# Performance work log

Measured on AMD Instinct MI355X. Metric: run time of the kernel, lower is better.

The kernel has to match this reference:

```python
import jax, jax.numpy as jnp
import numpy as np

N = 4000      # number_of_sensors
D_IN = 128    # input feature dim
D_OUT = 128   # output feature dim
E_DIM = 16    # node embedding dim
B = 8         # batch size


def setup_inputs() -> dict:
    key = jax.random.key(0)
    k_x, k_e1, k_e2, k_w = jax.random.split(key, 4)
    x = jax.random.normal(k_x, (B, N, D_IN), dtype=jnp.float32)
    E1 = jax.random.normal(k_e1, (N, E_DIM), dtype=jnp.float32)
    E2 = jax.random.normal(k_e2, (N, E_DIM), dtype=jnp.float32)
    W = jax.random.normal(k_w, (D_IN, D_OUT), dtype=jnp.float32) * (1.0 / np.sqrt(D_IN))
    b = jnp.zeros((D_OUT,), dtype=jnp.float32)
    return {"x": x, "E1": E1, "E2": E2, "W": W, "b": b}


def reference(x, E1, E2, W, b):
    # Adaptive adjacency from node embeddings: A = softmax(relu(E1 @ E2^T), axis=-1)
    logits = jax.nn.relu(jnp.einsum('nd,md->nm', E1, E2))  # [N, N]
    adj = jax.nn.softmax(logits, axis=-1)                  # row-normalized adjacency
    # Graph aggregation then feature transform: relu(A @ X @ W + b)
    agg = jnp.einsum('nm,bmf->bnf', adj, x)                # [B, N, D_IN]
    out = jax.nn.relu(jnp.einsum('bnf,fo->bno', agg, W) + b)  # [B, N, D_OUT]
    return out
```

## Files before the change

### kernel.cpp

```cpp
#include <hip/hip_runtime.h>
#include <hip/hip_bf16.h>

#define NSEN 4000
#define NP   4096
#define DIN  128
#define DOUT 128
#define EDIM 16
#define BATCH 8

typedef __attribute__((ext_vector_type(8))) short bf16x8;
typedef __attribute__((ext_vector_type(4))) float f32x4;

__device__ __forceinline__ unsigned short f2bf(float f) {
  unsigned int u = __float_as_uint(f);
  unsigned int r = (u + 0x7FFFu + ((u >> 16) & 1u)) >> 16;
  return (unsigned short)r;
}
__device__ __forceinline__ float bf2f(unsigned short s) {
  unsigned int u = ((unsigned int)s) << 16;
  return __uint_as_float(u);
}

__device__ __forceinline__ void gl_lds16(const void* g, void* l) {
  __builtin_amdgcn_global_load_lds((const __attribute__((address_space(1))) void*)g,
                                   (__attribute__((address_space(3))) void*)l, 16, 0, 0);
}

__global__ __launch_bounds__(512) void k_adj(const float* __restrict__ E1,
                                             const float* __restrict__ E2,
                                             const float* __restrict__ W,
                                             unsigned short* __restrict__ adjp,
                                             float* __restrict__ rinv,
                                             unsigned short* __restrict__ Wt) {
  __shared__ float rsum[8][16];
  if (blockIdx.x == NSEN / 16) {
    for (int i = threadIdx.x; i < DIN * DOUT; i += 512) {
      int o = i >> 7, f = i & 127;
      Wt[i] = f2bf(W[(size_t)f * DOUT + o]);
    }
    return;
  }
  const int tid = threadIdx.x;
  const int lane = tid & 63, wv = tid >> 6;
  const int lr = lane & 15, lq = lane >> 4;
  const int n0 = blockIdx.x * 16;

  float a[8];
  {
    const float* e1p = &E1[(size_t)(n0 + lr) * EDIM + (lq & 1) * 8];
    *(float4*)&a[0] = *(const float4*)e1p;
    *(float4*)&a[4] = *(const float4*)(e1p + 4);
  }
  bf16x8 af1, af2;
#pragma unroll
  for (int j = 0; j < 8; j++) {
    unsigned short hs = f2bf(a[j]);
    af1[j] = (short)hs;
    float lo = a[j] - bf2f(hs);
    af2[j] = (lq < 2) ? (short)f2bf(lo) : (short)0;
  }

  float rs[4] = {0.f, 0.f, 0.f, 0.f};
  for (int t = wv; t < NSEN / 16; t += 8) {
    const int m = t * 16 + lr;
    float bv[8];
    const float* e2p = &E2[(size_t)m * EDIM + (lq & 1) * 8];
    *(float4*)&bv[0] = *(const float4*)e2p;
    *(float4*)&bv[4] = *(const float4*)(e2p + 4);
    bf16x8 bfrag;
#pragma unroll
    for (int j = 0; j < 8; j++) {
      unsigned short hs = f2bf(bv[j]);
      if (lq < 2) bfrag[j] = (short)hs;
      else        bfrag[j] = (short)f2bf(bv[j] - bf2f(hs));
    }
    f32x4 c = (f32x4){0.f, 0.f, 0.f, 0.f};
    c = __builtin_amdgcn_mfma_f32_16x16x32_bf16(af1, bfrag, c, 0, 0, 0);
    c = __builtin_amdgcn_mfma_f32_16x16x32_bf16(af2, bfrag, c, 0, 0, 0);
#pragma unroll
    for (int i = 0; i < 4; i++) {
      float p = __expf(fmaxf(c[i], 0.f));
      rs[i] += p;
      adjp[(size_t)(n0 + lq * 4 + i) * NP + t * 16 + lr] = f2bf(p);
    }
  }
  for (int i = tid; i < 16 * (NP - NSEN); i += 512) {
    int r = i / (NP - NSEN), c = i % (NP - NSEN);
    adjp[(size_t)(n0 + r) * NP + NSEN + c] = 0;
  }
#pragma unroll
  for (int i = 0; i < 4; i++) {
    rs[i] += __shfl_xor(rs[i], 1, 64);
    rs[i] += __shfl_xor(rs[i], 2, 64);
    rs[i] += __shfl_xor(rs[i], 4, 64);
    rs[i] += __shfl_xor(rs[i], 8, 64);
  }
  if (lr == 0) {
#pragma unroll
    for (int i = 0; i < 4; i++) rsum[wv][lq * 4 + i] = rs[i];
  }
  __syncthreads();
  if (tid < 16) {
    float s = 0.f;
#pragma unroll
    for (int w = 0; w < 8; w++) s += rsum[w][tid];
    rinv[n0 + tid] = 1.0f / s;
  }
}

__global__ __launch_bounds__(256) void k_xpt(const float* __restrict__ x,
                                             unsigned short* __restrict__ xpt) {
  __shared__ unsigned short tile[64][72];
  const int t = threadIdx.x;
  const int m0 = blockIdx.x * 64;
  const int f0 = blockIdx.y * 64;
  const int b  = blockIdx.z;
  const int f4 = t & 15, mrow = t >> 4;
#pragma unroll
  for (int rep = 0; rep < 4; rep++) {
    int ml = mrow + rep * 16;
    int m = m0 + ml;
    float4 v = make_float4(0.f, 0.f, 0.f, 0.f);
    if (m < NSEN) v = *(const float4*)&x[((size_t)b * NSEN + m) * DIN + f0 + f4 * 4];
    tile[f4*4+0][ml] = f2bf(v.x);
    tile[f4*4+1][ml] = f2bf(v.y);
    tile[f4*4+2][ml] = f2bf(v.z);
    tile[f4*4+3][ml] = f2bf(v.w);
  }
  __syncthreads();
  const int seg = t & 7, fl0 = t >> 3;
#pragma unroll
  for (int it = 0; it < 2; it++) {
    int fl = fl0 + it * 32;
    int j = b * DIN + f0 + fl;
    uint4 v = *(const uint4*)&tile[fl][seg * 8];
    *(uint4*)&xpt[(size_t)j * NP + m0 + seg * 8] = v;
  }
}

__global__ __launch_bounds__(256, 2) void k_gemm1(const unsigned short* __restrict__ A,
                                                  const unsigned short* __restrict__ Bt,
                                                  const unsigned short* __restrict__ Wt,
                                                  const float* __restrict__ rinv,
                                                  const float* __restrict__ bias,
                                                  float* __restrict__ out) {
  __shared__ __align__(16) unsigned short smem[36864];
  const int tid = threadIdx.x;
  const int lane = tid & 63, wv = tid >> 6;
  const int wr = wv >> 1, wc = wv & 1;
  const int lr = lane & 15, lq = lane >> 4;
  const int m0 = blockIdx.x * 64;
  const int b  = blockIdx.y;
  const int c0 = b * 128;
  unsigned short* tA0 = smem;
  unsigned short* tB0 = smem + 12288;

  f32x4 acc[2][4];
#pragma unroll
  for (int p = 0; p < 2; p++)
#pragma unroll
    for (int q = 0; q < 4; q++) acc[p][q] = (f32x4){0.f, 0.f, 0.f, 0.f};

#define STAGE(bufi, kb)                                                              \
  {                                                                                  \
    _Pragma("unroll")                                                                \
    for (int s = 0; s < 2; s++) {                                                    \
      int idx = s * 256 + tid;                                                       \
      int row = idx >> 3;                                                            \
      int kc = ((idx & 7) ^ (row & 7)) << 3;                                         \
      gl_lds16(&A[(size_t)(m0 + row) * NP + (kb) + kc], &tA0[(bufi)*4096 + idx*8]);  \
    }                                                                                \
    _Pragma("unroll")                                                                \
    for (int s = 0; s < 4; s++) {                                                    \
      int idx = s * 256 + tid;                                                       \
      int row = idx >> 3;                                                            \
      int kc = ((idx & 7) ^ (row & 7)) << 3;                                         \
      gl_lds16(&Bt[(size_t)(c0 + row) * NP + (kb) + kc], &tB0[(bufi)*8192 + idx*8]); \
    }                                                                                \
  }

  STAGE(0, 0);
  STAGE(1, 64);

  int cur = 0;
  for (int it = 0; it < 64; ++it) {
    if (it < 62) {
      int nb = cur + 2; if (nb >= 3) nb -= 3;
      STAGE(nb, (it + 2) * 64);
      asm volatile("s_waitcnt vmcnt(12)" ::: "memory");
    } else if (it == 62) {
      asm volatile("s_waitcnt vmcnt(6)" ::: "memory");
    } else {
      asm volatile("s_waitcnt vmcnt(0)" ::: "memory");
    }
    __builtin_amdgcn_s_barrier();

    bf16x8 af[2][2], bfr[2][4];
#pragma unroll
    for (int sk = 0; sk < 2; sk++) {
      const int koff = (sk * 32 + lq * 8) ^ ((lr & 7) << 3);
#pragma unroll
      for (int p = 0; p < 2; p++)
        af[sk][p] = *(const bf16x8*)&tA0[cur * 4096 + (wr * 32 + p * 16 + lr) * 64 + koff];
#pragma unroll
      for (int q = 0; q < 4; q++)
        bfr[sk][q] = *(const bf16x8*)&tB0[cur * 8192 + (wc * 64 + q * 16 + lr) * 64 + koff];
    }
    asm volatile("s_waitcnt lgkmcnt(0)" ::: "memory");
    __builtin_amdgcn_sched_barrier(0);
    __builtin_amdgcn_s_setprio(1);
#pragma unroll
    for (int sk = 0; sk < 2; sk++)
#pragma unroll
      for (int p = 0; p < 2; p++)
#pragma unroll
        for (int q = 0; q < 4; q++)
          acc[p][q] = __builtin_amdgcn_mfma_f32_16x16x32_bf16(af[sk][p], bfr[sk][q], acc[p][q], 0, 0, 0);
    __builtin_amdgcn_s_setprio(0);
    __builtin_amdgcn_s_barrier();
    cur = cur + 1; if (cur >= 3) cur = 0;
  }
#undef STAGE

  bf16x8 wf[4][4];
#pragma unroll
  for (int q = 0; q < 4; q++)
#pragma unroll
    for (int ks = 0; ks < 4; ks++)
      wf[q][ks] = *(const bf16x8*)&Wt[(size_t)(wc * 64 + q * 16 + lr) * DIN + ks * 32 + lq * 8];

  unsigned short* eps = smem;
#pragma unroll
  for (int p = 0; p < 2; p++) {
    float rv[4];
#pragma unroll
    for (int i = 0; i < 4; i++)
      rv[i] = rinv[m0 + wr * 32 + p * 16 + lq * 4 + i];
#pragma unroll
    for (int q = 0; q < 4; q++)
#pragma unroll
      for (int i = 0; i < 4; i++)
        eps[(wr * 32 + p * 16 + lq * 4 + i) * 136 + wc * 64 + q * 16 + lr] =
            f2bf(acc[p][q][i] * rv[i]);
  }
  __syncthreads();

  f32x4 acc2[2][4];
#pragma unroll
  for (int p = 0; p < 2; p++)
#pragma unroll
    for (int q = 0; q < 4; q++) acc2[p][q] = (f32x4){0.f, 0.f, 0.f, 0.f};

#pragma unroll
  for (int ks = 0; ks < 4; ks++) {
    bf16x8 a2[2];
#pragma unroll
    for (int p = 0; p < 2; p++)
      a2[p] = *(const bf16x8*)&eps[(wr * 32 + p * 16 + lr) * 136 + ks * 32 + lq * 8];
#pragma unroll
    for (int p = 0; p < 2; p++)
#pragma unroll
      for (int q = 0; q < 4; q++)
        acc2[p][q] = __builtin_amdgcn_mfma_f32_16x16x32_bf16(a2[p], wf[q][ks], acc2[p][q], 0, 0, 0);
  }

#pragma unroll
  for (int p = 0; p < 2; p++)
#pragma unroll
    for (int q = 0; q < 4; q++) {
      const int o = wc * 64 + q * 16 + lr;
      const float bb = bias[o];
#pragma unroll
      for (int i = 0; i < 4; i++) {
        const int n = m0 + wr * 32 + p * 16 + lq * 4 + i;
        if (n < NSEN)
          out[((size_t)b * NSEN + n) * DOUT + o] = fmaxf(acc2[p][q][i] + bb, 0.f);
      }
    }
}

extern "C" void kernel_launch(void* const* d_in, const int* in_sizes, int n_in,
                              void* d_out, int out_size, void* d_ws, size_t ws_size,
                              hipStream_t stream) {
  const float* x    = (const float*)d_in[0];
  const float* E1   = (const float*)d_in[1];
  const float* E2   = (const float*)d_in[2];
  const float* W    = (const float*)d_in[3];
  const float* bias = (const float*)d_in[4];
  float* out = (float*)d_out;

  char* ws = (char*)d_ws;
  unsigned short* adjp = (unsigned short*)(ws);
  unsigned short* xpt  = (unsigned short*)(ws + 33554432);
  unsigned short* wt   = (unsigned short*)(ws + 33554432 + 8388608);
  float*          rinv = (float*)(ws + 33554432 + 8388608 + 32768);

  k_adj<<<dim3(NSEN / 16 + 1), dim3(512), 0, stream>>>(E1, E2, W, adjp, rinv, wt);
  k_xpt<<<dim3(NP / 64, DIN / 64, BATCH), dim3(256), 0, stream>>>(x, xpt);
  k_gemm1<<<dim3(NP / 64, BATCH), dim3(256), 0, stream>>>(adjp, xpt, wt, rinv, bias, out);
}
```

Baseline: 81.54 us.

## Split-K the adjacency GEMM into two halves with a separate reduce-and-project kernel

The main GEMM is split along K into two halves via a third grid dimension, so the launch grows from 8x64 to 2x8x63 blocks, improving CU occupancy on a 256-CU device. Each half writes bf16 partial sums to a workspace. A new finishing kernel adds the two partials, applies the row normalisation and runs the W projection, bias and relu. The pipeline drops from triple to double buffering, and LDS fragment loads are split so the first MFMA group can start early, allowing three blocks per CU. This costs an extra launch, partial-sum traffic and bf16 rounding of the partials. The grid now uses 63 row tiles instead of 64, which skips only padded rows beyond 4000.

```diff
diff --git a/kernel.cpp b/kernel.cpp
--- a/kernel.cpp
+++ b/kernel.cpp
@@ -138,22 +138,21 @@
   }
 }
 
-__global__ __launch_bounds__(256, 2) void k_gemm1(const unsigned short* __restrict__ A,
+__global__ __launch_bounds__(256, 3) void k_gemm1(const unsigned short* __restrict__ A,
                                                   const unsigned short* __restrict__ Bt,
-                                                  const unsigned short* __restrict__ Wt,
-                                                  const float* __restrict__ rinv,
-                                                  const float* __restrict__ bias,
-                                                  float* __restrict__ out) {
-  __shared__ __align__(16) unsigned short smem[36864];
+                                                  unsigned short* __restrict__ part) {
+  __shared__ __align__(16) unsigned short smem[24576];
   const int tid = threadIdx.x;
   const int lane = tid & 63, wv = tid >> 6;
   const int wr = wv >> 1, wc = wv & 1;
   const int lr = lane & 15, lq = lane >> 4;
   const int m0 = blockIdx.x * 64;
   const int b  = blockIdx.y;
+  const int kh = blockIdx.z;
   const int c0 = b * 128;
+  const int kb0 = kh * 2048;
   unsigned short* tA0 = smem;
-  unsigned short* tB0 = smem + 12288;
+  unsigned short* tB0 = smem + 8192;
 
   f32x4 acc[2][4];
 #pragma unroll
@@ -179,48 +178,86 @@
     }                                                                                \
   }
 
-  STAGE(0, 0);
-  STAGE(1, 64);
-
-  int cur = 0;
-  for (int it = 0; it < 64; ++it) {
-    if (it < 62) {
-      int nb = cur + 2; if (nb >= 3) nb -= 3;
-      STAGE(nb, (it + 2) * 64);
-      asm volatile("s_waitcnt vmcnt(12)" ::: "memory");
-    } else if (it == 62) {
+  STAGE(0, kb0);
+
+  for (int it = 0; it < 32; ++it) {
+    const int cur = it & 1;
+    if (it < 31) {
+      STAGE(cur ^ 1, kb0 + (it + 1) * 64);
       asm volatile("s_waitcnt vmcnt(6)" ::: "memory");
     } else {
       asm volatile("s_waitcnt vmcnt(0)" ::: "memory");
     }
     __builtin_amdgcn_s_barrier();
 
-    bf16x8 af[2][2], bfr[2][4];
-#pragma unroll
-    for (int sk = 0; sk < 2; sk++) {
-      const int koff = (sk * 32 + lq * 8) ^ ((lr & 7) << 3);
+    bf16x8 af0[2], bf0[4], af1[2], bf1[4];
+    {
+      const int koff0 = (lq * 8) ^ ((lr & 7) << 3);
 #pragma unroll
       for (int p = 0; p < 2; p++)
-        af[sk][p] = *(const bf16x8*)&tA0[cur * 4096 + (wr * 32 + p * 16 + lr) * 64 + koff];
-#pragma unroll
-      for (int q = 0; q < 4; q++)
-        bfr[sk][q] = *(const bf16x8*)&tB0[cur * 8192 + (wc * 64 + q * 16 + lr) * 64 + koff];
-    }
+        af0[p] = *(const bf16x8*)&tA0[cur * 4096 + (wr * 32 + p * 16 + lr) * 64 + koff0];
+#pragma unroll
+      for (int q = 0; q < 4; q++)
+        bf0[q] = *(const bf16x8*)&tB0[cur * 8192 + (wc * 64 + q * 16 + lr) * 64 + koff0];
+    }
+    __builtin_amdgcn_sched_barrier(0);
+    {
+      const int koff1 = (32 + lq * 8) ^ ((lr & 7) << 3);
+#pragma unroll
+      for (int p = 0; p < 2; p++)
+        af1[p] = *(const bf16x8*)&tA0[cur * 4096 + (wr * 32 + p * 16 + lr) * 64 + koff1];
+#pragma unroll
+      for (int q = 0; q < 4; q++)
+        bf1[q] = *(const bf16x8*)&tB0[cur * 8192 + (wc * 64 + q * 16 + lr) * 64 + koff1];
+    }
+    asm volatile("s_waitcnt lgkmcnt(6)" ::: "memory");
+    __builtin_amdgcn_sched_barrier(0);
+    __builtin_amdgcn_s_setprio(1);
+#pragma unroll
+    for (int p = 0; p < 2; p++)
+#pragma unroll
+      for (int q = 0; q < 4; q++)
+        acc[p][q] = __builtin_amdgcn_mfma_f32_16x16x32_bf16(af0[p], bf0[q], acc[p][q], 0, 0, 0);
     asm volatile("s_waitcnt lgkmcnt(0)" ::: "memory");
     __builtin_amdgcn_sched_barrier(0);
-    __builtin_amdgcn_s_setprio(1);
-#pragma unroll
-    for (int sk = 0; sk < 2; sk++)
-#pragma unroll
-      for (int p = 0; p < 2; p++)
-#pragma unroll
-        for (int q = 0; q < 4; q++)
-          acc[p][q] = __builtin_amdgcn_mfma_f32_16x16x32_bf16(af[sk][p], bfr[sk][q], acc[p][q], 0, 0, 0);
+#pragma unroll
+    for (int p = 0; p < 2; p++)
+#pragma unroll
+      for (int q = 0; q < 4; q++)
+        acc[p][q] = __builtin_amdgcn_mfma_f32_16x16x32_bf16(af1[p], bf1[q], acc[p][q], 0, 0, 0);
     __builtin_amdgcn_s_setprio(0);
     __builtin_amdgcn_s_barrier();
-    cur = cur + 1; if (cur >= 3) cur = 0;
   }
 #undef STAGE
+
+  unsigned short* pdst = part + ((size_t)(kh * BATCH + b) * NP + m0) * DIN;
+#pragma unroll
+  for (int p = 0; p < 2; p++)
+#pragma unroll
+    for (int q = 0; q < 4; q++) {
+      const int col = wc * 64 + q * 16 + lr;
+#pragma unroll
+      for (int i = 0; i < 4; i++) {
+        const int row = wr * 32 + p * 16 + lq * 4 + i;
+        pdst[row * DIN + col] = f2bf(acc[p][q][i]);
+      }
+    }
+}
+
+__global__ __launch_bounds__(256, 2) void k_fin(const unsigned short* __restrict__ part,
+                                                const unsigned short* __restrict__ Wt,
+                                                const float* __restrict__ rinv,
+                                                const float* __restrict__ bias,
+                                                float* __restrict__ out) {
+  __shared__ __align__(16) unsigned short eps[64 * 136];
+  const int tid = threadIdx.x;
+  const int lane = tid & 63, wv = tid >> 6;
+  const int wr = wv >> 1, wc = wv & 1;
+  const int lr = lane & 15, lq = lane >> 4;
+  const int m0 = blockIdx.x * 64;
+  const int b = blockIdx.y;
+  const size_t base = ((size_t)b * NP + m0) * DIN;
+  const size_t khoff = (size_t)BATCH * NP * DIN;
 
   bf16x8 wf[4][4];
 #pragma unroll
@@ -229,19 +266,18 @@
     for (int ks = 0; ks < 4; ks++)
       wf[q][ks] = *(const bf16x8*)&Wt[(size_t)(wc * 64 + q * 16 + lr) * DIN + ks * 32 + lq * 8];
 
-  unsigned short* eps = smem;
-#pragma unroll
-  for (int p = 0; p < 2; p++) {
-    float rv[4];
-#pragma unroll
-    for (int i = 0; i < 4; i++)
-      rv[i] = rinv[m0 + wr * 32 + p * 16 + lq * 4 + i];
-#pragma unroll
-    for (int q = 0; q < 4; q++)
-#pragma unroll
-      for (int i = 0; i < 4; i++)
-        eps[(wr * 32 + p * 16 + lq * 4 + i) * 136 + wc * 64 + q * 16 + lr] =
-            f2bf(acc[p][q][i] * rv[i]);
+#pragma unroll
+  for (int s = 0; s < 4; s++) {
+    int c = s * 256 + tid;
+    int row = c >> 4, col = (c & 15) * 8;
+    bf16x8 p0 = *(const bf16x8*)&part[base + row * DIN + col];
+    bf16x8 p1 = *(const bf16x8*)&part[khoff + base + row * DIN + col];
+    float rv = rinv[m0 + row];
+    unsigned short tmp[8];
+#pragma unroll
+    for (int j = 0; j < 8; j++)
+      tmp[j] = f2bf((bf2f((unsigned short)p0[j]) + bf2f((unsigned short)p1[j])) * rv);
+    *(bf16x8*)&eps[row * 136 + col] = *(bf16x8*)tmp;
   }
   __syncthreads();
 
@@ -294,8 +330,10 @@
   unsigned short* xpt  = (unsigned short*)(ws + 33554432);
   unsigned short* wt   = (unsigned short*)(ws + 33554432 + 8388608);
   float*          rinv = (float*)(ws + 33554432 + 8388608 + 32768);
+  unsigned short* part = (unsigned short*)(ws + 33554432 + 8388608 + 32768 + 16384);
 
   k_adj<<<dim3(NSEN / 16 + 1), dim3(512), 0, stream>>>(E1, E2, W, adjp, rinv, wt);
   k_xpt<<<dim3(NP / 64, DIN / 64, BATCH), dim3(256), 0, stream>>>(x, xpt);
-  k_gemm1<<<dim3(NP / 64, BATCH), dim3(256), 0, stream>>>(adjp, xpt, wt, rinv, bias, out);
-}
+  k_gemm1<<<dim3(63, BATCH, 2), dim3(256), 0, stream>>>(adjp, xpt, part);
+  k_fin<<<dim3(63, BATCH), dim3(256), 0, stream>>>(part, wt, rinv, bias, out);
+}
```

New measurement: 95.15 us. 1.17x slower.

## Use 8-wave blocks with double-buffered LDS and split-K MFMA interleave

Applied to the files above, without the earlier changes.

The main GEMM kernel moves from 4 waves to 8 waves per block, so each wave owns a 32x32 output sub-tile. The LDS pipeline drops from triple to double buffering, which shrinks shared memory and allows more resident blocks. LDS fragment loads are split into two k-halves so MFMAs on the first half can start while the second half is still loading. The trade-off is a shallower global prefetch (one stage ahead instead of two) and more barrier participants per block, in exchange for higher occupancy and better latency hiding.

```diff
diff --git a/kernel.cpp b/kernel.cpp
--- a/kernel.cpp
+++ b/kernel.cpp
@@ -138,41 +138,40 @@
   }
 }
 
-__global__ __launch_bounds__(256, 2) void k_gemm1(const unsigned short* __restrict__ A,
+__global__ __launch_bounds__(512, 4) void k_gemm1(const unsigned short* __restrict__ A,
                                                   const unsigned short* __restrict__ Bt,
                                                   const unsigned short* __restrict__ Wt,
                                                   const float* __restrict__ rinv,
                                                   const float* __restrict__ bias,
                                                   float* __restrict__ out) {
-  __shared__ __align__(16) unsigned short smem[36864];
+  __shared__ __align__(16) unsigned short smem[24576];
   const int tid = threadIdx.x;
   const int lane = tid & 63, wv = tid >> 6;
-  const int wr = wv >> 1, wc = wv & 1;
+  const int wr = wv >> 2, wc = wv & 3;
   const int lr = lane & 15, lq = lane >> 4;
   const int m0 = blockIdx.x * 64;
   const int b  = blockIdx.y;
   const int c0 = b * 128;
   unsigned short* tA0 = smem;
-  unsigned short* tB0 = smem + 12288;
-
-  f32x4 acc[2][4];
+  unsigned short* tB0 = smem + 8192;
+
+  f32x4 acc[2][2];
 #pragma unroll
   for (int p = 0; p < 2; p++)
 #pragma unroll
-    for (int q = 0; q < 4; q++) acc[p][q] = (f32x4){0.f, 0.f, 0.f, 0.f};
+    for (int q = 0; q < 2; q++) acc[p][q] = (f32x4){0.f, 0.f, 0.f, 0.f};
 
 #define STAGE(bufi, kb)                                                              \
   {                                                                                  \
-    _Pragma("unroll")                                                                \
-    for (int s = 0; s < 2; s++) {                                                    \
-      int idx = s * 256 + tid;                                                       \
+    {                                                                                \
+      int idx = tid;                                                                 \
       int row = idx >> 3;                                                            \
       int kc = ((idx & 7) ^ (row & 7)) << 3;                                         \
       gl_lds16(&A[(size_t)(m0 + row) * NP + (kb) + kc], &tA0[(bufi)*4096 + idx*8]);  \
     }                                                                                \
     _Pragma("unroll")                                                                \
-    for (int s = 0; s < 4; s++) {                                                    \
-      int idx = s * 256 + tid;                                                       \
+    for (int s = 0; s < 2; s++) {                                                    \
+      int idx = s * 512 + tid;                                                       \
       int row = idx >> 3;                                                            \
       int kc = ((idx & 7) ^ (row & 7)) << 3;                                         \
       gl_lds16(&Bt[(size_t)(c0 + row) * NP + (kb) + kc], &tB0[(bufi)*8192 + idx*8]); \
@@ -180,54 +179,63 @@
   }
 
   STAGE(0, 0);
-  STAGE(1, 64);
-
-  int cur = 0;
+
   for (int it = 0; it < 64; ++it) {
-    if (it < 62) {
-      int nb = cur + 2; if (nb >= 3) nb -= 3;
-      STAGE(nb, (it + 2) * 64);
-      asm volatile("s_waitcnt vmcnt(12)" ::: "memory");
-    } else if (it == 62) {
-      asm volatile("s_waitcnt vmcnt(6)" ::: "memory");
+    const int cur = it & 1;
+    if (it < 63) {
+      STAGE(cur ^ 1, (it + 1) * 64);
+      asm volatile("s_waitcnt vmcnt(3)" ::: "memory");
     } else {
       asm volatile("s_waitcnt vmcnt(0)" ::: "memory");
     }
     __builtin_amdgcn_s_barrier();
 
-    bf16x8 af[2][2], bfr[2][4];
-#pragma unroll
-    for (int sk = 0; sk < 2; sk++) {
-      const int koff = (sk * 32 + lq * 8) ^ ((lr & 7) << 3);
+    bf16x8 af0[2], bf0[2], af1[2], bf1[2];
+    {
+      const int koff0 = (lq * 8) ^ ((lr & 7) << 3);
 #pragma unroll
       for (int p = 0; p < 2; p++)
-        af[sk][p] = *(const bf16x8*)&tA0[cur * 4096 + (wr * 32 + p * 16 + lr) * 64 + koff];
-#pragma unroll
-      for (int q = 0; q < 4; q++)
-        bfr[sk][q] = *(const bf16x8*)&tB0[cur * 8192 + (wc * 64 + q * 16 + lr) * 64 + koff];
-    }
+        af0[p] = *(const bf16x8*)&tA0[cur * 4096 + (wr * 32 + p * 16 + lr) * 64 + koff0];
+#pragma unroll
+      for (int q = 0; q < 2; q++)
+        bf0[q] = *(const bf16x8*)&tB0[cur * 8192 + (wc * 32 + q * 16 + lr) * 64 + koff0];
+    }
+    __builtin_amdgcn_sched_barrier(0);
+    {
+      const int koff1 = (32 + lq * 8) ^ ((lr & 7) << 3);
+#pragma unroll
+      for (int p = 0; p < 2; p++)
+        af1[p] = *(const bf16x8*)&tA0[cur * 4096 + (wr * 32 + p * 16 + lr) * 64 + koff1];
+#pragma unroll
+      for (int q = 0; q < 2; q++)
+        bf1[q] = *(const bf16x8*)&tB0[cur * 8192 + (wc * 32 + q * 16 + lr) * 64 + koff1];
+    }
+    asm volatile("s_waitcnt lgkmcnt(4)" ::: "memory");
+    __builtin_amdgcn_sched_barrier(0);
+    __builtin_amdgcn_s_setprio(1);
+#pragma unroll
+    for (int p = 0; p < 2; p++)
+#pragma unroll
+      for (int q = 0; q < 2; q++)
+        acc[p][q] = __builtin_amdgcn_mfma_f32_16x16x32_bf16(af0[p], bf0[q], acc[p][q], 0, 0, 0);
     asm volatile("s_waitcnt lgkmcnt(0)" ::: "memory");
     __builtin_amdgcn_sched_barrier(0);
-    __builtin_amdgcn_s_setprio(1);
-#pragma unroll
-    for (int sk = 0; sk < 2; sk++)
-#pragma unroll
-      for (int p = 0; p < 2; p++)
-#pragma unroll
-        for (int q = 0; q < 4; q++)
-          acc[p][q] = __builtin_amdgcn_mfma_f32_16x16x32_bf16(af[sk][p], bfr[sk][q], acc[p][q], 0, 0, 0);
+#pragma unroll
+    for (int p = 0; p < 2; p++)
+#pragma unroll
+      for (int q = 0; q < 2; q++)
+        acc[p][q] = __builtin_amdgcn_mfma_f32_16x16x32_bf16(af1[p], bf1[q], acc[p][q], 0, 0, 0);
     __builtin_amdgcn_s_setprio(0);
     __builtin_amdgcn_s_barrier();
-    cur = cur + 1; if (cur >= 3) cur = 0;
   }
 #undef STAGE
 
-  bf16x8 wf[4][4];
-#pragma unroll
-  for (int q = 0; q < 4; q++)
+  bf16x8 wf[2][4];
+#pragma unroll
+  for (int q = 0; q < 2; q++)
 #pragma unroll
     for (int ks = 0; ks < 4; ks++)
-      wf[q][ks] = *(const bf16x8*)&Wt[(size_t)(wc * 64 + q * 16 + lr) * DIN + ks * 32 + lq * 8];
+      wf[q][ks] = *(const bf16x8*)&Wt[(size_t)(wc * 32 + q * 16 + lr) * DIN + ks * 32 + lq * 8];
 
   unsigned short* eps = smem;
 #pragma unroll
@@ -237,19 +245,19 @@
     for (int i = 0; i < 4; i++)
       rv[i] = rinv[m0 + wr * 32 + p * 16 + lq * 4 + i];
 #pragma unroll
-    for (int q = 0; q < 4; q++)
+    for (int q = 0; q < 2; q++)
 #pragma unroll
       for (int i = 0; i < 4; i++)
-        eps[(wr * 32 + p * 16 + lq * 4 + i) * 136 + wc * 64 + q * 16 + lr] =
+        eps[(wr * 32 + p * 16 + lq * 4 + i) * 136 + wc * 32 + q * 16 + lr] =
             f2bf(acc[p][q][i] * rv[i]);
   }
   __syncthreads();
 
-  f32x4 acc2[2][4];
+  f32x4 acc2[2][2];
 #pragma unroll
   for (int p = 0; p < 2; p++)
 #pragma unroll
-    for (int q = 0; q < 4; q++) acc2[p][q] = (f32x4){0.f, 0.f, 0.f, 0.f};
+    for (int q = 0; q < 2; q++) acc2[p][q] = (f32x4){0.f, 0.f, 0.f, 0.f};
 
 #pragma unroll
   for (int ks = 0; ks < 4; ks++) {
@@ -260,15 +268,15 @@
 #pragma unroll
     for (int p = 0; p < 2; p++)
 #pragma unroll
-      for (int q = 0; q < 4; q++)
+      for (int q = 0; q < 2; q++)
         acc2[p][q] = __builtin_amdgcn_mfma_f32_16x16x32_bf16(a2[p], wf[q][ks], acc2[p][q], 0, 0, 0);
   }
 
 #pragma unroll
   for (int p = 0; p < 2; p++)
 #pragma unroll
-    for (int q = 0; q < 4; q++) {
-      const int o = wc * 64 + q * 16 + lr;
+    for (int q = 0; q < 2; q++) {
+      const int o = wc * 32 + q * 16 + lr;
       const float bb = bias[o];
 #pragma unroll
       for (int i = 0; i < 4; i++) {
@@ -297,5 +305,5 @@
 
   k_adj<<<dim3(NSEN / 16 + 1), dim3(512), 0, stream>>>(E1, E2, W, adjp, rinv, wt);
   k_xpt<<<dim3(NP / 64, DIN / 64, BATCH), dim3(256), 0, stream>>>(x, xpt);
-  k_gemm1<<<dim3(NP / 64, BATCH), dim3(256), 0, stream>>>(adjp, xpt, wt, rinv, bias, out);
-}
+  k_gemm1<<<dim3(NP / 64, BATCH), dim3(512), 0, stream>>>(adjp, xpt, wt, rinv, bias, out);
+}
```

After: 80.61 us. No clear change (-1.1%).
